# Kernel optimization log

Hardware: AMD Instinct MI355X
Metric: run time of the kernel (lower is better)

## Reference

```python
import jax, jax.numpy as jnp
import numpy as np

L = 16384          # leaves of complete binary tree
D = 256            # word_dim == tree_input_dim == output_dim
V = 50257          # num_words
NL = 5             # num_labels


def setup_inputs() -> dict:
    key = jax.random.key(0)
    ks = jax.random.split(key, 8)
    s = 0.05
    return {
        "tokens": jax.random.randint(ks[0], (L,), 0, V),
        "emb": jax.random.normal(ks[1], (V, D), jnp.float32) * s,      # word_embedding.weight
        "Wx": jax.random.normal(ks[2], (D, 5 * D), jnp.float32) * s,   # input->gates (leaf only)
        "Ul": jax.random.normal(ks[3], (D, 5 * D), jnp.float32) * s,   # left-child h -> gates
        "Ur": jax.random.normal(ks[4], (D, 5 * D), jnp.float32) * s,   # right-child h -> gates
        "b": jnp.zeros((5 * D,), jnp.float32),
        "Wp": jax.random.normal(ks[5], (D, NL), jnp.float32) * s,      # pred_layer
        "bp": jnp.zeros((NL,), jnp.float32),
    }


def _cell(pre, c_l, c_r):
    # Binary TreeLSTM cell: gates [i, f_l, f_r, o, u]
    i, fl, fr, o, u = jnp.split(pre, 5, axis=-1)
    c = jax.nn.sigmoid(i) * jnp.tanh(u) + jax.nn.sigmoid(fl) * c_l + jax.nn.sigmoid(fr) * c_r
    h = jax.nn.sigmoid(o) * jnp.tanh(c)
    return h, c


def reference(tokens, emb, Wx, Ul, Ur, b, Wp, bp):
    # dropout layers are identity at inference (no-op here)
    x = emb[tokens]                                  # [L, D] seq_output == word embeddings (leaf_rnn=False)
    # leaf nodes: l/r child states are zeros, inputs = seq_out[idx]
    h, c = _cell(x @ Wx + b, 0.0, 0.0)               # [L, D]
    hs = [h]
    # internal nodes level by level (complete binary tree): inputs=None -> no Wx term
    while h.shape[0] > 1:
        hl, hr = h[0::2], h[1::2]
        cl, cr = c[0::2], c[1::2]
        h, c = _cell(hl @ Ul + hr @ Ur + b, cl, cr)
        hs.append(h)
    hidden = jnp.concatenate(hs, axis=0)             # [2L-1, D] all node hidden states
    return hidden @ Wp + bp                          # single_h_pred logits [2L-1, NL]
```

## Files before the change

kernel.cpp:

```cpp
#include <hip/hip_runtime.h>
#include <hip/hip_bf16.h>
#include <math.h>
#include <stdint.h>


typedef __attribute__((ext_vector_type(8))) short     bf16x8;
typedef __attribute__((ext_vector_type(4))) float     f32x4;
typedef __attribute__((ext_vector_type(8))) unsigned short u16x8;

#define NGATE 5

__device__ __forceinline__ uint16_t f2bf(float f) {
    uint32_t u = __builtin_bit_cast(uint32_t, f);
    u = (u + 0x7fffu + ((u >> 16) & 1u)) >> 16;
    return (uint16_t)u;
}
__device__ __forceinline__ float bf2f(uint16_t h) {
    uint32_t u = ((uint32_t)h) << 16;
    return __builtin_bit_cast(float, u);
}
__device__ __forceinline__ float sigf(float x) { return 1.0f / (1.0f + __expf(-x)); }
__device__ __forceinline__ float tanhfast(float x) {
    float e = __expf(2.0f * x);
    return (e - 1.0f) / (e + 1.0f);
}

__device__ __forceinline__ void gld_lds16(const void* g, void* l) {
    __builtin_amdgcn_global_load_lds(
        (const __attribute__((address_space(1))) void*)g,
        (__attribute__((address_space(3))) void*)l,
        16, 0, 0);
}

__global__ __launch_bounds__(256) void pack_w_kernel(
    const float* __restrict__ W0, const float* __restrict__ W1, int KT,
    uint16_t* __restrict__ dhi, uint16_t* __restrict__ dlo)
{
    int gid = blockIdx.x * 256 + threadIdx.x;
    int total = 80 * KT * 64;
    if (gid >= total) return;
    int lane = gid & 63;
    int n  = ((gid >> 6) / KT) * 16 + (lane & 15);
    int kt = (gid >> 6) % KT;
    int k0 = kt * 32 + (lane >> 4) * 8;
    u16x8 vh, vl;
    #pragma unroll
    for (int j = 0; j < 8; ++j) {
        int k = k0 + j;
        const float* src = (k < 256) ? (W0 + (size_t)k * 1280)
                                     : (W1 + (size_t)(k - 256) * 1280);
        float v = src[n];
        uint16_t h = f2bf(v);
        vh[j] = h;
        vl[j] = f2bf(v - bf2f(h));
    }
    *(u16x8*)(dhi + (size_t)gid * 8) = vh;
    *(u16x8*)(dlo + (size_t)gid * 8) = vl;
}

template<int BM, int KT, int JT, bool LVL0>
__global__ __launch_bounds__(256) void lvl_gemm(
    const uint16_t* __restrict__ Ahi, const uint16_t* __restrict__ Alo,
    const int* __restrict__ tokens, const float* __restrict__ emb,
    const uint16_t* __restrict__ Bhi, const uint16_t* __restrict__ Blo,
    const float* __restrict__ b,
    const float* __restrict__ c_prev,
    uint16_t* __restrict__ h_hi_out, uint16_t* __restrict__ h_lo_out,
    float* __restrict__ c_out, int n)
{
    constexpr int K   = KT * 32;
    constexpr int MT  = BM / 64;
    constexpr int NC  = NGATE * JT * 2;

    __shared__ __align__(16) uint16_t sB0[NC * 512];
    __shared__ __align__(16) uint16_t sB1[NC * 512];

    const int tid  = threadIdx.x;
    const int wave = tid >> 6;
    const int lane = tid & 63;
    const int quad = lane >> 4;
    const int l15  = lane & 15;
    const int r0   = blockIdx.x * BM;
    const int jn   = blockIdx.y;

    f32x4 acc[MT][JT][NGATE] = {};

    const uint16_t* aph[MT];
    const uint16_t* apl[MT];
    const float*    ebase[MT];
    #pragma unroll
    for (int mt = 0; mt < MT; ++mt) {
        int row = r0 + (wave * MT + mt) * 16 + l15;
        row = min(row, n - 1);
        if constexpr (LVL0) {
            int tok = tokens[row];
            ebase[mt] = emb + (size_t)tok * 256 + quad * 8;
        } else {
            aph[mt] = Ahi + (size_t)row * K + quad * 8;
            apl[mt] = Alo + (size_t)row * K + quad * 8;
        }
    }

    auto stageB = [&](uint16_t* dB, int kt) {
        #pragma unroll
        for (int c = wave; c < NC; c += 4) {
            int hl = c & 1, gj = c >> 1;
            const uint16_t* src = hl ? Blo : Bhi;
            int nt = (gj / JT) * 16 + jn * JT + (gj % JT);
            gld_lds16(src + ((size_t)(nt * KT + kt) * 64 + lane) * 8,
                      dB + c * 512);
        }
    };
    auto loadAn = [&](bf16x8 (&ah)[MT], bf16x8 (&al)[MT], int kt) {
        #pragma unroll
        for (int mt = 0; mt < MT; ++mt) {
            ah[mt] = *(const bf16x8*)(aph[mt] + kt * 32);
            al[mt] = *(const bf16x8*)(apl[mt] + kt * 32);
        }
    };
    auto loadA0 = [&](float4 (&e)[MT][2], int kt) {
        #pragma unroll
        for (int mt = 0; mt < MT; ++mt) {
            const float4* p = (const float4*)(ebase[mt] + kt * 32);
            e[mt][0] = p[0];
            e[mt][1] = p[1];
        }
    };
    auto cvtA0 = [&](const float4 (&e)[MT][2], bf16x8 (&ah)[MT], bf16x8 (&al)[MT]) {
        #pragma unroll
        for (int mt = 0; mt < MT; ++mt) {
            float fv[8];
            fv[0] = e[mt][0].x; fv[1] = e[mt][0].y; fv[2] = e[mt][0].z; fv[3] = e[mt][0].w;
            fv[4] = e[mt][1].x; fv[5] = e[mt][1].y; fv[6] = e[mt][1].z; fv[7] = e[mt][1].w;
            #pragma unroll
            for (int j = 0; j < 8; ++j) {
                uint16_t h = f2bf(fv[j]);
                ah[mt][j] = (short)h;
                al[mt][j] = (short)f2bf(fv[j] - bf2f(h));
            }
        }
    };
    auto mfma_all = [&](const bf16x8 (&ah)[MT], const bf16x8 (&al)[MT],
                        const uint16_t* Bx) {
        #pragma unroll
        for (int g = 0; g < NGATE; ++g) {
            #pragma unroll
            for (int js = 0; js < JT; ++js) {
                const uint16_t* bp = Bx + (g * JT + js) * 1024;
                bf16x8 bh = *(const bf16x8*)(bp + lane * 8);
                bf16x8 bl = *(const bf16x8*)(bp + 512 + lane * 8);
                #pragma unroll
                for (int mt = 0; mt < MT; ++mt) {
                    acc[mt][js][g] = __builtin_amdgcn_mfma_f32_16x16x32_bf16(ah[mt], bh, acc[mt][js][g], 0, 0, 0);
                    acc[mt][js][g] = __builtin_amdgcn_mfma_f32_16x16x32_bf16(al[mt], bh, acc[mt][js][g], 0, 0, 0);
                    acc[mt][js][g] = __builtin_amdgcn_mfma_f32_16x16x32_bf16(ah[mt], bl, acc[mt][js][g], 0, 0, 0);
                }
            }
        }
    };

    if constexpr (LVL0) {
        float4 eA[MT][2], eB[MT][2];
        loadA0(eA, 0);
        stageB(sB0, 0);
        __syncthreads();
        for (int kt = 0; kt < KT; kt += 2) {
            loadA0(eB, kt + 1);
            stageB(sB1, kt + 1);
            {
                bf16x8 ah[MT], al[MT];
                cvtA0(eA, ah, al);
                mfma_all(ah, al, sB0);
            }
            __syncthreads();
            if (kt + 2 < KT) { loadA0(eA, kt + 2); stageB(sB0, kt + 2); }
            {
                bf16x8 ah[MT], al[MT];
                cvtA0(eB, ah, al);
                mfma_all(ah, al, sB1);
            }
            __syncthreads();
        }
    } else {
        bf16x8 hA[MT], lA[MT], hB[MT], lB[MT];
        loadAn(hA, lA, 0);
        stageB(sB0, 0);
        __syncthreads();
        for (int kt = 0; kt < KT; kt += 2) {
            loadAn(hB, lB, kt + 1);
            stageB(sB1, kt + 1);
            mfma_all(hA, lA, sB0);
            __syncthreads();
            if (kt + 2 < KT) { loadAn(hA, lA, kt + 2); stageB(sB0, kt + 2); }
            mfma_all(hB, lB, sB1);
            __syncthreads();
        }
    }

    const int d0 = (jn * JT) * 16 + l15;
    float bg[JT][NGATE];
    #pragma unroll
    for (int js = 0; js < JT; ++js)
        #pragma unroll
        for (int g = 0; g < NGATE; ++g) bg[js][g] = b[g * 256 + d0 + js * 16];

    #pragma unroll
    for (int mt = 0; mt < MT; ++mt) {
        int rb = r0 + wave * (MT * 16) + mt * 16 + quad * 4;
        #pragma unroll
        for (int v = 0; v < 4; ++v) {
            int row = rb + v;
            if (row < n) {
                #pragma unroll
                for (int js = 0; js < JT; ++js) {
                    int d = d0 + js * 16;
                    float gi = acc[mt][js][0][v] + bg[js][0];
                    float fl = acc[mt][js][1][v] + bg[js][1];
                    float fr = acc[mt][js][2][v] + bg[js][2];
                    float go = acc[mt][js][3][v] + bg[js][3];
                    float gu = acc[mt][js][4][v] + bg[js][4];
                    float cc;
                    if constexpr (LVL0) {
                        cc = sigf(gi) * tanhfast(gu);
                        (void)fl; (void)fr;
                    } else {
                        float cl = c_prev[(size_t)(2 * row) * 256 + d];
                        float cr = c_prev[(size_t)(2 * row + 1) * 256 + d];
                        cc = sigf(gi) * tanhfast(gu) + sigf(fl) * cl + sigf(fr) * cr;
                    }
                    float hh = sigf(go) * tanhfast(cc);
                    uint16_t hb = f2bf(hh);
                    h_hi_out[(size_t)row * 256 + d] = hb;
                    h_lo_out[(size_t)row * 256 + d] = f2bf(hh - bf2f(hb));
                    c_out[(size_t)row * 256 + d] = cc;
                }
            }
        }
    }
}

__global__ __launch_bounds__(256) void proj_kernel(
    const uint16_t* __restrict__ h_hi, const uint16_t* __restrict__ h_lo,
    const float* __restrict__ Wp, const float* __restrict__ bp,
    float* __restrict__ out, int n)
{
    const int wave = blockIdx.x * 4 + (threadIdx.x >> 6);
    const int lane = threadIdx.x & 63;
    if (wave >= n) return;

    const uint16_t* hh = h_hi + (size_t)wave * 256;
    const uint16_t* hl = h_lo + (size_t)wave * 256;
    float s[5] = {0.f, 0.f, 0.f, 0.f, 0.f};
    #pragma unroll
    for (int q = 0; q < 4; ++q) {
        int dd = lane + 64 * q;
        float hv = bf2f(hh[dd]) + bf2f(hl[dd]);
        #pragma unroll
        for (int j = 0; j < 5; ++j) s[j] += hv * Wp[dd * 5 + j];
    }
    #pragma unroll
    for (int off = 32; off; off >>= 1)
        #pragma unroll
        for (int j = 0; j < 5; ++j) s[j] += __shfl_down(s[j], off);

    if (lane == 0) {
        #pragma unroll
        for (int j = 0; j < 5; ++j) out[(size_t)wave * 5 + j] = s[j] + bp[j];
    }
}

extern "C" void kernel_launch(void* const* d_in, const int* in_sizes, int n_in,
                              void* d_out, int out_size, void* d_ws, size_t ws_size,
                              hipStream_t stream)
{
    const int*   tokens = (const int*)  d_in[0];
    const float* emb    = (const float*)d_in[1];
    const float* Wx     = (const float*)d_in[2];
    const float* Ul     = (const float*)d_in[3];
    const float* Ur     = (const float*)d_in[4];
    const float* b      = (const float*)d_in[5];
    const float* Wp     = (const float*)d_in[6];
    const float* bp     = (const float*)d_in[7];
    float* out = (float*)d_out;

    uint8_t* w = (uint8_t*)d_ws;
    uint16_t* h_hi = (uint16_t*)w;  w += (size_t)32767 * 256 * 2;
    uint16_t* h_lo = (uint16_t*)w;  w += (size_t)32767 * 256 * 2;
    float*    cA   = (float*)w;     w += (size_t)16384 * 256 * 4;
    float*    cB   = (float*)w;     w += (size_t)8192  * 256 * 4;
    uint16_t* BxH  = (uint16_t*)w;  w += (size_t)80 * 8  * 64 * 8 * 2;
    uint16_t* BxL  = (uint16_t*)w;  w += (size_t)80 * 8  * 64 * 8 * 2;
    uint16_t* BuH  = (uint16_t*)w;  w += (size_t)80 * 16 * 64 * 8 * 2;
    uint16_t* BuL  = (uint16_t*)w;  w += (size_t)80 * 16 * 64 * 8 * 2;

    pack_w_kernel<<<(80 * 8  * 64) / 256, 256, 0, stream>>>(Wx, Wx, 8,  BxH, BxL);
    pack_w_kernel<<<(80 * 16 * 64) / 256, 256, 0, stream>>>(Ul, Ur, 16, BuH, BuL);

    int off[16];
    off[0] = 0;
    for (int t = 0; t < 15; ++t) off[t + 1] = off[t] + (16384 >> t);

    lvl_gemm<128, 8, 2, true><<<dim3(16384 / 128, 8), 256, 0, stream>>>(
        nullptr, nullptr, tokens, emb, BxH, BxL, b, nullptr,
        h_hi, h_lo, cA, 16384);

    for (int t = 1; t <= 14; ++t) {
        int n = 16384 >> t;
        const uint16_t* Ah = h_hi + (size_t)off[t - 1] * 256;
        const uint16_t* Al = h_lo + (size_t)off[t - 1] * 256;
        float* c_in  = (t % 2 == 0) ? cB : cA;
        float* c_out = (t % 2 == 0) ? cA : cB;
        uint16_t* Hh = h_hi + (size_t)off[t] * 256;
        uint16_t* Hl = h_lo + (size_t)off[t] * 256;
        if (n >= 4096) {
            lvl_gemm<128, 16, 2, false><<<dim3(n / 128, 8), 256, 0, stream>>>(
                Ah, Al, nullptr, nullptr, BuH, BuL, b, c_in, Hh, Hl, c_out, n);
        } else if (n >= 2048) {
            lvl_gemm<64, 16, 2, false><<<dim3(n / 64, 8), 256, 0, stream>>>(
                Ah, Al, nullptr, nullptr, BuH, BuL, b, c_in, Hh, Hl, c_out, n);
        } else {
            int gx = (n + 63) / 64; if (gx < 1) gx = 1;
            lvl_gemm<64, 16, 1, false><<<dim3(gx, 16), 256, 0, stream>>>(
                Ah, Al, nullptr, nullptr, BuH, BuL, b, c_in, Hh, Hl, c_out, n);
        }
    }

    int total = off[15];
    proj_kernel<<<(total + 3) / 4, 256, 0, stream>>>(h_hi, h_lo, Wp, bp, out, total);
}
```

Before: 340.3 us.

## Fuse tree levels 3-14 into one cooperative persistent kernel with grid sync

Levels 3 through 14 of the tree, where row counts shrink, now run in a single cooperative kernel launched with 256 blocks of 512 threads. Each wave takes 16x16 output tiles, reads A and the packed weights straight from global memory, and runs the hi/lo split bf16 MFMA. A grid.sync separates consecutive levels. This removes a dozen small kernel launches and the under-filled GPU on tiny levels, at the cost of no LDS reuse of B and the overhead of grid-wide barriers. If the cooperative launch fails, the code falls back to the per-level launches.

```diff
diff --git a/kernel.cpp b/kernel.cpp
--- a/kernel.cpp
+++ b/kernel.cpp
@@ -1,7 +1,10 @@
 #include <hip/hip_runtime.h>
 #include <hip/hip_bf16.h>
+#include <hip/hip_cooperative_groups.h>
 #include <math.h>
 #include <stdint.h>
+
+namespace cg = cooperative_groups;
 
 
 typedef __attribute__((ext_vector_type(8))) short     bf16x8;
@@ -9,6 +12,7 @@
 typedef __attribute__((ext_vector_type(8))) unsigned short u16x8;
 
 #define NGATE 5
+#define TAIL_T0 3
 
 __device__ __forceinline__ uint16_t f2bf(float f) {
     uint32_t u = __builtin_bit_cast(uint32_t, f);
@@ -102,7 +106,6 @@
     }
 
     auto stageB = [&](uint16_t* dB, int kt) {
-        #pragma unroll
         for (int c = wave; c < NC; c += 4) {
             int hl = c & 1, gj = c >> 1;
             const uint16_t* src = hl ? Blo : Bhi;
@@ -239,6 +242,98 @@
     }
 }
 
+__global__ __launch_bounds__(512) void tail_kernel(
+    const uint16_t* __restrict__ BuH, const uint16_t* __restrict__ BuL,
+    const float* __restrict__ bias,
+    uint16_t* __restrict__ h_hi, uint16_t* __restrict__ h_lo,
+    float* __restrict__ cA, float* __restrict__ cB, int t0)
+{
+    cg::grid_group grid = cg::this_grid();
+    const int lane = threadIdx.x & 63;
+    const int quad = lane >> 4;
+    const int l15  = lane & 15;
+    const int gw   = blockIdx.x * 8 + (threadIdx.x >> 6);
+    const int nw   = gridDim.x * 8;
+
+    for (int t = t0; t <= 14; ++t) {
+        const int n = 16384 >> t;
+        const size_t offp = 32768 - (32768 >> (t - 1));
+        const size_t offc = 32768 - (32768 >> t);
+        const uint16_t* Ah = h_hi + offp * 256;
+        const uint16_t* Al = h_lo + offp * 256;
+        const float* c_in  = (t & 1) ? cA : cB;
+        float*       c_out = (t & 1) ? cB : cA;
+        const int mtiles = (n + 15) >> 4;
+
+        for (int tile = gw; tile < mtiles * 16; tile += nw) {
+            const int mt = tile >> 4;
+            const int jn = tile & 15;
+            int rowa = mt * 16 + l15;
+            if (rowa > n - 1) rowa = n - 1;
+            const uint16_t* ap = Ah + (size_t)rowa * 512 + quad * 8;
+            const uint16_t* lp = Al + (size_t)rowa * 512 + quad * 8;
+            const uint16_t* bH = BuH + (size_t)jn * 8192 + lane * 8;
+            const uint16_t* bL = BuL + (size_t)jn * 8192 + lane * 8;
+
+            f32x4 acc[NGATE] = {};
+            bf16x8 ah0, al0, ah1, al1;
+            bf16x8 bh0[NGATE], bl0[NGATE], bh1[NGATE], bl1[NGATE];
+
+            auto ld = [&](bf16x8& ah, bf16x8& al,
+                          bf16x8 (&bh)[NGATE], bf16x8 (&bl)[NGATE], int kt) {
+                ah = *(const bf16x8*)(ap + kt * 32);
+                al = *(const bf16x8*)(lp + kt * 32);
+                #pragma unroll
+                for (int g = 0; g < NGATE; ++g) {
+                    bh[g] = *(const bf16x8*)(bH + (size_t)g * 131072 + kt * 512);
+                    bl[g] = *(const bf16x8*)(bL + (size_t)g * 131072 + kt * 512);
+                }
+            };
+            auto step = [&](const bf16x8& ah, const bf16x8& al,
+                            const bf16x8 (&bh)[NGATE], const bf16x8 (&bl)[NGATE]) {
+                #pragma unroll
+                for (int g = 0; g < NGATE; ++g) {
+                    acc[g] = __builtin_amdgcn_mfma_f32_16x16x32_bf16(ah, bh[g], acc[g], 0, 0, 0);
+                    acc[g] = __builtin_amdgcn_mfma_f32_16x16x32_bf16(al, bh[g], acc[g], 0, 0, 0);
+                    acc[g] = __builtin_amdgcn_mfma_f32_16x16x32_bf16(ah, bl[g], acc[g], 0, 0, 0);
+                }
+            };
+
+            ld(ah0, al0, bh0, bl0, 0);
+            #pragma unroll
+            for (int kt = 0; kt < 16; kt += 2) {
+                ld(ah1, al1, bh1, bl1, kt + 1);
+                step(ah0, al0, bh0, bl0);
+                if (kt + 2 < 16) ld(ah0, al0, bh0, bl0, kt + 2);
+                step(ah1, al1, bh1, bl1);
+            }
+
+            const int d = jn * 16 + l15;
+            #pragma unroll
+            for (int v = 0; v < 4; ++v) {
+                int row = mt * 16 + quad * 4 + v;
+                if (row < n) {
+                    float gi = acc[0][v] + bias[0 * 256 + d];
+                    float fl = acc[1][v] + bias[1 * 256 + d];
+                    float fr = acc[2][v] + bias[2 * 256 + d];
+                    float go = acc[3][v] + bias[3 * 256 + d];
+                    float gu = acc[4][v] + bias[4 * 256 + d];
+                    float cl = c_in[(size_t)(2 * row) * 256 + d];
+                    float cr = c_in[(size_t)(2 * row + 1) * 256 + d];
+                    float cc = sigf(gi) * tanhfast(gu) + sigf(fl) * cl + sigf(fr) * cr;
+                    float hh = sigf(go) * tanhfast(cc);
+                    uint16_t hb = f2bf(hh);
+                    h_hi[(offc + row) * 256 + d] = hb;
+                    h_lo[(offc + row) * 256 + d] = f2bf(hh - bf2f(hb));
+                    c_out[(size_t)row * 256 + d] = cc;
+                }
+            }
+        }
+        __threadfence();
+        if (t < 14) grid.sync();
+    }
+}
+
 __global__ __launch_bounds__(256) void proj_kernel(
     const uint16_t* __restrict__ h_hi, const uint16_t* __restrict__ h_lo,
     const float* __restrict__ Wp, const float* __restrict__ bp,
@@ -304,7 +399,7 @@
         nullptr, nullptr, tokens, emb, BxH, BxL, b, nullptr,
         h_hi, h_lo, cA, 16384);
 
-    for (int t = 1; t <= 14; ++t) {
+    for (int t = 1; t < TAIL_T0; ++t) {
         int n = 16384 >> t;
         const uint16_t* Ah = h_hi + (size_t)off[t - 1] * 256;
         const uint16_t* Al = h_lo + (size_t)off[t - 1] * 256;
@@ -312,16 +407,36 @@
         float* c_out = (t % 2 == 0) ? cA : cB;
         uint16_t* Hh = h_hi + (size_t)off[t] * 256;
         uint16_t* Hl = h_lo + (size_t)off[t] * 256;
-        if (n >= 4096) {
-            lvl_gemm<128, 16, 2, false><<<dim3(n / 128, 8), 256, 0, stream>>>(
-                Ah, Al, nullptr, nullptr, BuH, BuL, b, c_in, Hh, Hl, c_out, n);
-        } else if (n >= 2048) {
-            lvl_gemm<64, 16, 2, false><<<dim3(n / 64, 8), 256, 0, stream>>>(
-                Ah, Al, nullptr, nullptr, BuH, BuL, b, c_in, Hh, Hl, c_out, n);
-        } else {
-            int gx = (n + 63) / 64; if (gx < 1) gx = 1;
-            lvl_gemm<64, 16, 1, false><<<dim3(gx, 16), 256, 0, stream>>>(
-                Ah, Al, nullptr, nullptr, BuH, BuL, b, c_in, Hh, Hl, c_out, n);
+        lvl_gemm<128, 16, 2, false><<<dim3(n / 128, 8), 256, 0, stream>>>(
+            Ah, Al, nullptr, nullptr, BuH, BuL, b, c_in, Hh, Hl, c_out, n);
+    }
+
+    {
+        int t0 = TAIL_T0;
+        void* targs[] = { (void*)&BuH, (void*)&BuL, (void*)&b,
+                          (void*)&h_hi, (void*)&h_lo,
+                          (void*)&cA, (void*)&cB, (void*)&t0 };
+        hipError_t e = hipLaunchCooperativeKernel(
+            (const void*)tail_kernel, dim3(256), dim3(512), targs, 0, stream);
+        if (e != hipSuccess) {
+            (void)hipGetLastError();
+            for (int t = TAIL_T0; t <= 14; ++t) {
+                int n = 16384 >> t;
+                const uint16_t* Ah = h_hi + (size_t)off[t - 1] * 256;
+                const uint16_t* Al = h_lo + (size_t)off[t - 1] * 256;
+                float* c_in  = (t % 2 == 0) ? cB : cA;
+                float* c_out = (t % 2 == 0) ? cA : cB;
+                uint16_t* Hh = h_hi + (size_t)off[t] * 256;
+                uint16_t* Hl = h_lo + (size_t)off[t] * 256;
+                if (n >= 2048) {
+                    lvl_gemm<64, 16, 2, false><<<dim3(n / 64, 8), 256, 0, stream>>>(
+                        Ah, Al, nullptr, nullptr, BuH, BuL, b, c_in, Hh, Hl, c_out, n);
+                } else {
+                    int gx = (n + 63) / 64; if (gx < 1) gx = 1;
+                    lvl_gemm<64, 16, 1, false><<<dim3(gx, 16), 256, 0, stream>>>(
+                        Ah, Al, nullptr, nullptr, BuH, BuL, b, c_in, Hh, Hl, c_out, n);
+                }
+            }
         }
     }
 
```

New measurement: 1.213 ms. +256.5%, slower.

## Add split-K register-resident tail kernel for small tree levels

Applied to the files above, without the earlier changes.

Adds a new tail_lvl kernel for levels with n at or below 2048 rows. Each block handles 32 rows and 16 output columns across all five gates. The four waves split the K dimension, load A and B fragments straight from global memory into registers with no LDS staging, and reduce partial sums through shared memory before wave 0 runs the cell epilogue. This is meant to raise parallelism and cut per-level latency on the small, latency-bound upper levels, at the cost of more B traffic per block and an extra reduction step. It also drops an unroll pragma in stageB.

```diff
diff --git a/kernel.cpp b/kernel.cpp
--- a/kernel.cpp
+++ b/kernel.cpp
@@ -9,6 +9,7 @@
 typedef __attribute__((ext_vector_type(8))) unsigned short u16x8;
 
 #define NGATE 5
+#define TAIL_T0 3
 
 __device__ __forceinline__ uint16_t f2bf(float f) {
     uint32_t u = __builtin_bit_cast(uint32_t, f);
@@ -102,7 +103,6 @@
     }
 
     auto stageB = [&](uint16_t* dB, int kt) {
-        #pragma unroll
         for (int c = wave; c < NC; c += 4) {
             int hl = c & 1, gj = c >> 1;
             const uint16_t* src = hl ? Blo : Bhi;
@@ -239,6 +239,141 @@
     }
 }
 
+struct TailFrags {
+    bf16x8 a0h, a0l, a1h, a1l;
+    bf16x8 b0h, b1h, b2h, b3h, b4h;
+    bf16x8 b0l, b1l, b2l, b3l, b4l;
+};
+
+#define TL_LOAD(F, KTG) do {                                                  \
+    F.a0h = *(const bf16x8*)(a0hp + (KTG) * 32);                              \
+    F.a0l = *(const bf16x8*)(a0lp + (KTG) * 32);                              \
+    F.a1h = *(const bf16x8*)(a1hp + (KTG) * 32);                              \
+    F.a1l = *(const bf16x8*)(a1lp + (KTG) * 32);                              \
+    F.b0h = *(const bf16x8*)(bHp + 0 * 131072 + (KTG) * 512);                 \
+    F.b1h = *(const bf16x8*)(bHp + 1 * 131072 + (KTG) * 512);                 \
+    F.b2h = *(const bf16x8*)(bHp + 2 * 131072 + (KTG) * 512);                 \
+    F.b3h = *(const bf16x8*)(bHp + 3 * 131072 + (KTG) * 512);                 \
+    F.b4h = *(const bf16x8*)(bHp + 4 * 131072 + (KTG) * 512);                 \
+    F.b0l = *(const bf16x8*)(bLp + 0 * 131072 + (KTG) * 512);                 \
+    F.b1l = *(const bf16x8*)(bLp + 1 * 131072 + (KTG) * 512);                 \
+    F.b2l = *(const bf16x8*)(bLp + 2 * 131072 + (KTG) * 512);                 \
+    F.b3l = *(const bf16x8*)(bLp + 3 * 131072 + (KTG) * 512);                 \
+    F.b4l = *(const bf16x8*)(bLp + 4 * 131072 + (KTG) * 512);                 \
+} while (0)
+
+#define TL_MM3(ACC, AH, AL, BH, BL2)                                          \
+    ACC = __builtin_amdgcn_mfma_f32_16x16x32_bf16(AH, BH, ACC, 0, 0, 0);      \
+    ACC = __builtin_amdgcn_mfma_f32_16x16x32_bf16(AL, BH, ACC, 0, 0, 0);      \
+    ACC = __builtin_amdgcn_mfma_f32_16x16x32_bf16(AH, BL2, ACC, 0, 0, 0);
+
+#define TL_STEP(F) do {                                                       \
+    TL_MM3(acc00, F.a0h, F.a0l, F.b0h, F.b0l)                                 \
+    TL_MM3(acc01, F.a0h, F.a0l, F.b1h, F.b1l)                                 \
+    TL_MM3(acc02, F.a0h, F.a0l, F.b2h, F.b2l)                                 \
+    TL_MM3(acc03, F.a0h, F.a0l, F.b3h, F.b3l)                                 \
+    TL_MM3(acc04, F.a0h, F.a0l, F.b4h, F.b4l)                                 \
+    TL_MM3(acc10, F.a1h, F.a1l, F.b0h, F.b0l)                                 \
+    TL_MM3(acc11, F.a1h, F.a1l, F.b1h, F.b1l)                                 \
+    TL_MM3(acc12, F.a1h, F.a1l, F.b2h, F.b2l)                                 \
+    TL_MM3(acc13, F.a1h, F.a1l, F.b3h, F.b3l)                                 \
+    TL_MM3(acc14, F.a1h, F.a1l, F.b4h, F.b4l)                                 \
+} while (0)
+
+#define TL_RST(M, G, A) {                                                     \
+    r[(M)*20 + (G)*4 + 0] = A[0]; r[(M)*20 + (G)*4 + 1] = A[1];               \
+    r[(M)*20 + (G)*4 + 2] = A[2]; r[(M)*20 + (G)*4 + 3] = A[3]; }
+
+#define TL_RADD(M, G, A) {                                                    \
+    A[0] += r[(M)*20 + (G)*4 + 0]; A[1] += r[(M)*20 + (G)*4 + 1];             \
+    A[2] += r[(M)*20 + (G)*4 + 2]; A[3] += r[(M)*20 + (G)*4 + 3]; }
+
+#define TL_EPI(M, A0, A1, A2, A3, A4) do {                                    \
+    int rb = (mt0 + (M)) * 16 + quad * 4;                                     \
+    _Pragma("unroll")                                                         \
+    for (int v = 0; v < 4; ++v) {                                             \
+        int row = rb + v;                                                     \
+        if (row < n) {                                                        \
+            float gi = A0[v] + bias[0 * 256 + d];                             \
+            float fl = A1[v] + bias[1 * 256 + d];                             \
+            float fr = A2[v] + bias[2 * 256 + d];                             \
+            float go = A3[v] + bias[3 * 256 + d];                             \
+            float gu = A4[v] + bias[4 * 256 + d];                             \
+            float cl = c_in[(size_t)(2 * row) * 256 + d];                     \
+            float cr = c_in[(size_t)(2 * row + 1) * 256 + d];                 \
+            float cc = sigf(gi) * tanhfast(gu) + sigf(fl) * cl + sigf(fr) * cr; \
+            float hhv = sigf(go) * tanhfast(cc);                              \
+            uint16_t hb = f2bf(hhv);                                          \
+            hh_out[(size_t)row * 256 + d] = hb;                               \
+            hl_out[(size_t)row * 256 + d] = f2bf(hhv - bf2f(hb));             \
+            c_out[(size_t)row * 256 + d] = cc;                                \
+        }                                                                     \
+    }                                                                         \
+} while (0)
+
+__global__ __launch_bounds__(256) void tail_lvl(
+    const uint16_t* __restrict__ Ah, const uint16_t* __restrict__ Al,
+    const uint16_t* __restrict__ BuH, const uint16_t* __restrict__ BuL,
+    const float* __restrict__ bias, const float* __restrict__ c_in,
+    uint16_t* __restrict__ hh_out, uint16_t* __restrict__ hl_out,
+    float* __restrict__ c_out, int n)
+{
+    __shared__ float red[3][64][41];
+
+    const int tid  = threadIdx.x;
+    const int wave = tid >> 6;
+    const int lane = tid & 63;
+    const int quad = lane >> 4;
+    const int l15  = lane & 15;
+    const int mt0  = blockIdx.x * 2;
+    const int jn   = blockIdx.y;
+
+    int row0 = mt0 * 16 + l15;        if (row0 > n - 1) row0 = n - 1;
+    int row1 = (mt0 + 1) * 16 + l15;  if (row1 > n - 1) row1 = n - 1;
+    const uint16_t* a0hp = Ah + (size_t)row0 * 512 + quad * 8;
+    const uint16_t* a0lp = Al + (size_t)row0 * 512 + quad * 8;
+    const uint16_t* a1hp = Ah + (size_t)row1 * 512 + quad * 8;
+    const uint16_t* a1lp = Al + (size_t)row1 * 512 + quad * 8;
+    const uint16_t* bHp  = BuH + (size_t)jn * 8192 + lane * 8;
+    const uint16_t* bLp  = BuL + (size_t)jn * 8192 + lane * 8;
+    const int kb = wave * 4;
+
+    f32x4 acc00 = {}, acc01 = {}, acc02 = {}, acc03 = {}, acc04 = {};
+    f32x4 acc10 = {}, acc11 = {}, acc12 = {}, acc13 = {}, acc14 = {};
+
+    TailFrags f0, f1;
+    TL_LOAD(f0, kb + 0);
+    TL_LOAD(f1, kb + 1);
+    TL_STEP(f0);
+    TL_LOAD(f0, kb + 2);
+    TL_STEP(f1);
+    TL_LOAD(f1, kb + 3);
+    TL_STEP(f0);
+    TL_STEP(f1);
+
+    if (wave != 0) {
+        float* r = &red[wave - 1][lane][0];
+        TL_RST(0, 0, acc00) TL_RST(0, 1, acc01) TL_RST(0, 2, acc02)
+        TL_RST(0, 3, acc03) TL_RST(0, 4, acc04)
+        TL_RST(1, 0, acc10) TL_RST(1, 1, acc11) TL_RST(1, 2, acc12)
+        TL_RST(1, 3, acc13) TL_RST(1, 4, acc14)
+    }
+    __syncthreads();
+    if (wave == 0) {
+        #pragma unroll
+        for (int k = 0; k < 3; ++k) {
+            const float* r = &red[k][lane][0];
+            TL_RADD(0, 0, acc00) TL_RADD(0, 1, acc01) TL_RADD(0, 2, acc02)
+            TL_RADD(0, 3, acc03) TL_RADD(0, 4, acc04)
+            TL_RADD(1, 0, acc10) TL_RADD(1, 1, acc11) TL_RADD(1, 2, acc12)
+            TL_RADD(1, 3, acc13) TL_RADD(1, 4, acc14)
+        }
+        const int d = jn * 16 + l15;
+        TL_EPI(0, acc00, acc01, acc02, acc03, acc04);
+        TL_EPI(1, acc10, acc11, acc12, acc13, acc14);
+    }
+}
+
 __global__ __launch_bounds__(256) void proj_kernel(
     const uint16_t* __restrict__ h_hi, const uint16_t* __restrict__ h_lo,
     const float* __restrict__ Wp, const float* __restrict__ bp,
@@ -304,25 +439,30 @@
         nullptr, nullptr, tokens, emb, BxH, BxL, b, nullptr,
         h_hi, h_lo, cA, 16384);
 
-    for (int t = 1; t <= 14; ++t) {
+    for (int t = 1; t < TAIL_T0; ++t) {
         int n = 16384 >> t;
-        const uint16_t* Ah = h_hi + (size_t)off[t - 1] * 256;
-        const uint16_t* Al = h_lo + (size_t)off[t - 1] * 256;
+        const uint16_t* Ahp = h_hi + (size_t)off[t - 1] * 256;
+        const uint16_t* Alp = h_lo + (size_t)off[t - 1] * 256;
         float* c_in  = (t % 2 == 0) ? cB : cA;
         float* c_out = (t % 2 == 0) ? cA : cB;
         uint16_t* Hh = h_hi + (size_t)off[t] * 256;
         uint16_t* Hl = h_lo + (size_t)off[t] * 256;
-        if (n >= 4096) {
-            lvl_gemm<128, 16, 2, false><<<dim3(n / 128, 8), 256, 0, stream>>>(
-                Ah, Al, nullptr, nullptr, BuH, BuL, b, c_in, Hh, Hl, c_out, n);
-        } else if (n >= 2048) {
-            lvl_gemm<64, 16, 2, false><<<dim3(n / 64, 8), 256, 0, stream>>>(
-                Ah, Al, nullptr, nullptr, BuH, BuL, b, c_in, Hh, Hl, c_out, n);
-        } else {
-            int gx = (n + 63) / 64; if (gx < 1) gx = 1;
-            lvl_gemm<64, 16, 1, false><<<dim3(gx, 16), 256, 0, stream>>>(
-                Ah, Al, nullptr, nullptr, BuH, BuL, b, c_in, Hh, Hl, c_out, n);
-        }
+        lvl_gemm<128, 16, 2, false><<<dim3(n / 128, 8), 256, 0, stream>>>(
+            Ahp, Alp, nullptr, nullptr, BuH, BuL, b, c_in, Hh, Hl, c_out, n);
+    }
+
+    for (int t = TAIL_T0; t <= 14; ++t) {
+        int n = 16384 >> t;
+        const uint16_t* Ahp = h_hi + (size_t)off[t - 1] * 256;
+        const uint16_t* Alp = h_lo + (size_t)off[t - 1] * 256;
+        float* c_in  = (t % 2 == 0) ? cB : cA;
+        float* c_out = (t % 2 == 0) ? cA : cB;
+        uint16_t* Hh = h_hi + (size_t)off[t] * 256;
+        uint16_t* Hl = h_lo + (size_t)off[t] * 256;
+        int mtiles = (n + 15) >> 4;
+        int gx = (mtiles + 1) >> 1;
+        tail_lvl<<<dim3(gx, 16), 256, 0, stream>>>(
+            Ahp, Alp, BuH, BuL, b, c_in, Hh, Hl, c_out, n);
     }
 
     int total = off[15];
```

Measured after the change: 331.6 us. 1.03x faster.
